# Kernel tuning notes

Hardware: AMD Instinct MI355X
Metric: run time of the kernel (lower is better)

The kernel has to match this reference:

```python
import jax, jax.numpy as jnp
import numpy as np
from jax import lax

H = 65  # hidden size

def lstm_layer(x, w_ih, w_hh, b_ih, b_hh):
    # x: [B, T, in]; w_ih: [4H, in]; w_hh: [4H, H]; PyTorch gate order i,f,g,o
    B = x.shape[0]
    # precompute input contribution for all timesteps: [T, B, 4H]
    pre = jnp.einsum('bti,gi->tbg', x, w_ih) + (b_ih + b_hh)
    wh = w_hh.T  # [H, 4H]

    def step(carry, pre_t):
        h, c = carry
        gates = pre_t + h @ wh
        i, f, g, o = jnp.split(gates, 4, axis=-1)
        i = jax.nn.sigmoid(i)
        f = jax.nn.sigmoid(f)
        g = jnp.tanh(g)
        o = jax.nn.sigmoid(o)
        c = f * c + i * g
        h = o * jnp.tanh(c)
        return (h, c), h

    init = (jnp.zeros((B, H), x.dtype), jnp.zeros((B, H), x.dtype))
    _, hs = lax.scan(step, init, pre)  # hs: [T, B, H]
    return jnp.transpose(hs, (1, 0, 2))  # [B, T, H]


def setup_inputs() -> dict:
    key = jax.random.key(0)
    ks = jax.random.split(key, 11)
    B, T = 512, 1024
    s = 1.0 / np.sqrt(H)
    d = {
        'x': jax.random.normal(ks[0], (B, T, H), jnp.float32),
        'w_ih0': jax.random.normal(ks[1], (4 * H, H), jnp.float32) * s,
        'w_hh0': jax.random.normal(ks[2], (4 * H, H), jnp.float32) * s,
        'b_ih0': jax.random.normal(ks[3], (4 * H,), jnp.float32) * s,
        'b_hh0': jax.random.normal(ks[4], (4 * H,), jnp.float32) * s,
        'w_ih1': jax.random.normal(ks[5], (4 * H, H), jnp.float32) * s,
        'w_hh1': jax.random.normal(ks[6], (4 * H, H), jnp.float32) * s,
        'b_ih1': jax.random.normal(ks[7], (4 * H,), jnp.float32) * s,
        'b_hh1': jax.random.normal(ks[8], (4 * H,), jnp.float32) * s,
        'w_lin': jax.random.normal(ks[9], (1, H), jnp.float32) * s,
        'b_lin': jax.random.normal(ks[10], (1,), jnp.float32) * s,
    }
    return d


def reference(x, w_ih0, w_hh0, b_ih0, b_hh0, w_ih1, w_hh1, b_ih1, b_hh1, w_lin, b_lin):
    h1 = lstm_layer(x, w_ih0, w_hh0, b_ih0, b_hh0)   # [B, T, H]
    h2 = lstm_layer(h1, w_ih1, w_hh1, b_ih1, b_hh1)  # [B, T, H]
    last = h2[:, -1, :]                               # [B, H]
    return last @ w_lin.T + b_lin                     # [B, 1]
```

## Files before the change

### kernel.cpp

```cpp
#include <hip/hip_runtime.h>

#define H 65
#define T_STEPS 1024

typedef _Float16 half_t;
typedef _Float16 half2_t __attribute__((ext_vector_type(2)));

static __device__ __forceinline__ float dot2(half2_t a, half2_t b, float c) {
#if __has_builtin(__builtin_amdgcn_fdot2)
  return __builtin_amdgcn_fdot2(a, b, c, false);
#else
  float d;
  asm("v_dot2_f32_f16 %0, %1, %2, %3" : "=v"(d) : "v"(a), "v"(b), "v"(c));
  return d;
#endif
}

template <int CTRL>
static __device__ __forceinline__ float qperm(float v) {
  int r = __builtin_amdgcn_update_dpp(0, __builtin_bit_cast(int, v), CTRL, 0xF, 0xF, true);
  return __builtin_bit_cast(float, r);
}

template <int PAT>
static __device__ __forceinline__ float swz(float v) {
  int r = __builtin_amdgcn_ds_swizzle(__builtin_bit_cast(int, v), PAT);
  return __builtin_bit_cast(float, r);
}

#define LOG2E 1.44269504089f
static __device__ __forceinline__ float fast_sigm(float v) {
  float e = __builtin_amdgcn_exp2f(-LOG2E * v);
  return __builtin_amdgcn_rcpf(1.f + e);
}

static __device__ __forceinline__ float pick(int idx, float a, float b, float c, float d) {
  float lo = (idx & 1) ? b : a;
  float hi = (idx & 1) ? d : c;
  return (idx & 2) ? hi : lo;
}

__global__
__attribute__((amdgpu_flat_work_group_size(1024, 1024)))
__attribute__((amdgpu_waves_per_eu(4, 4)))
void lstm_fused(
    const float* __restrict__ x,
    const float* __restrict__ wih0, const float* __restrict__ whh0,
    const float* __restrict__ bih0, const float* __restrict__ bhh0,
    const float* __restrict__ wih1, const float* __restrict__ whh1,
    const float* __restrict__ bih1, const float* __restrict__ bhh1,
    const float* __restrict__ wlin, const float* __restrict__ blin,
    float* __restrict__ out)
{
  __shared__ __align__(16) half_t xh[2][2][2][144];
  __shared__ float h1f[2][H];

  const int tid = threadIdx.x;
  const int rr  = tid >> 9;
  const int t5  = tid & 511;
  const int b   = 2 * blockIdx.x + rr;

  const int quad = t5 >> 2;
  const int l  = (quad >= 65) ? 1 : 0;
  const int j  = quad - 65 * l;
  const int kh = (t5 >> 1) & 1;
  const int g0 = t5 & 1;
  const bool gz = (g0 == 0);
  const float mreg = gz ? 2.f : 1.f;
  const float msub = mreg - 1.f;

  half2_t w[2][33];
  float hb[2];
  {
    const float* wi = l ? wih1 : wih0;
    const float* wh = l ? whh1 : whh0;
    const float* bi = l ? bih1 : bih0;
    const float* bh = l ? bhh1 : bhh0;
#pragma unroll
    for (int cc = 0; cc < 2; ++cc) {
      const int row = (g0 + 2 * cc) * H + j;
      hb[cc] = 0.5f * (bi[row] + bh[row]);
      const float* src = (kh ? wh : wi) + row * H;
#pragma unroll
      for (int pp = 0; pp < 33; ++pp) {
        float e0 = src[2 * pp];
        float e1 = (2 * pp + 1 < H) ? src[2 * pp + 1] : 0.f;
        half2_t v = {(half_t)e0, (half_t)e1};
        w[cc][pp] = v;
      }
    }
  }

  const bool isW7 = (t5 >= 448);
  const int  w7   = t5 - 448;
  const int  ec   = w7 >> 3;
  const int  ck   = w7 & 7;
  const int  side = ck >> 2;
  const int  sck  = ck & 3;
  const int  ecoff = side * 144 + 36 * sck;
  half2_t ecw[9];
  float ecbias = 0.f;
  float cec = 0.f;
  if (isW7) {
    const int gec = ec & 3;
    const int jec = 63 + (ec >> 2);
    const int row = gec * H + jec;
    const float* src = (side ? whh1 : wih1) + row * H;
#pragma unroll
    for (int i = 0; i < 9; ++i) {
      int es = 9 * sck + i;
      float e0 = (es < 33) ? src[2 * es] : 0.f;
      float e1 = (es < 33 && 2 * es + 1 < H) ? src[2 * es + 1] : 0.f;
      half2_t v = {(half_t)e0, (half_t)e1};
      ecw[i] = v;
    }
    if (ck == 0) ecbias = bih1[row] + bhh1[row];
  } else {
#pragma unroll
    for (int i = 0; i < 9; ++i) {
      half2_t z = {(half_t)0.f, (half_t)0.f};
      ecw[i] = z;
    }
  }

  const bool isW6 = (t5 >= 384) && (t5 < 448);
  const int  u    = t5 - 384;

  for (int i = tid; i < 2 * 2 * 2 * 144; i += 1024) ((half_t*)xh)[i] = (half_t)0.f;
  __syncthreads();

  const float* xrow = x + (size_t)b * (size_t)(T_STEPS * H);
  float nxA = 0.f, nxB = 0.f;
  if (isW6) {
    xh[rr][0][0][u] = (half_t)xrow[u];
    if (u == 0) xh[rr][0][0][64] = (half_t)xrow[64];
    nxA = xrow[H + u];
    if (u == 0) nxB = xrow[H + 64];
  }
  __syncthreads();

  float cst = 0.f;

  for (int s = 0; s <= T_STEPS; ++s) {
    const int p = s & 1;

    float fA = 0.f, fB = 0.f;
    if (isW6 && (s + 2 < T_STEPS)) {
      const float* xr = xrow + (size_t)(s + 2) * H;
      fA = xr[u];
      if (u == 0) fB = xr[64];
    }

    const bool act = l ? (s >= 1) : (s < T_STEPS);
    if (act) {
      const half_t* xb = &xh[rr][l][p][0] + 72 * kh;
      float a0 = hb[0], a1 = hb[1];
#pragma unroll
      for (int c = 0; c < 8; ++c) {
        uint4 qv = ((const uint4*)xb)[c];
        half2_t x0 = __builtin_bit_cast(half2_t, qv.x);
        half2_t x1 = __builtin_bit_cast(half2_t, qv.y);
        half2_t x2 = __builtin_bit_cast(half2_t, qv.z);
        half2_t x3 = __builtin_bit_cast(half2_t, qv.w);
        a0 = dot2(x0, w[0][4 * c + 0], a0);
        a1 = dot2(x0, w[1][4 * c + 0], a1);
        a0 = dot2(x1, w[0][4 * c + 1], a0);
        a1 = dot2(x1, w[1][4 * c + 1], a1);
        a0 = dot2(x2, w[0][4 * c + 2], a0);
        a1 = dot2(x2, w[1][4 * c + 2], a1);
        a0 = dot2(x3, w[0][4 * c + 3], a0);
        a1 = dot2(x3, w[1][4 * c + 3], a1);
      }
      {
        half2_t xt = *(const half2_t*)(xb + 64);
        a0 = dot2(xt, w[0][32], a0);
        a1 = dot2(xt, w[1][32], a1);
      }
      a0 += qperm<0x4E>(a0);
      a1 += qperm<0x4E>(a1);
      float e0 = fast_sigm(a0);
      float e1 = mreg * fast_sigm(mreg * a1) - msub;
      float p0 = qperm<0xB1>(e0);
      float p1 = qperm<0xB1>(e1);
      float iv = gz ? e0 : p0;
      float fv = gz ? p0 : e0;
      float gv = gz ? e1 : p1;
      float ov = gz ? p1 : e1;
      cst = fv * cst + iv * gv;
      float th = 2.f * fast_sigm(2.f * cst) - 1.f;
      float hv = ov * th;
      if ((t5 & 3) == 0) {
        half_t hh = (half_t)hv;
        if (l == 0) {
          xh[rr][0][p ^ 1][72 + j] = hh;
          xh[rr][1][p ^ 1][j]      = hh;
        } else {
          xh[rr][1][p ^ 1][72 + j] = hh;
          if (s == T_STEPS) h1f[rr][j] = hv;
        }
      }
    }

    if (isW7 && s >= 1) {
      const char* xb1 = (const char*)&xh[rr][1][p][0];
      float aec = ecbias;
#pragma unroll
      for (int i = 0; i < 9; ++i) {
        unsigned qv = *(const unsigned*)(xb1 + ecoff + 4 * i);
        aec = dot2(__builtin_bit_cast(half2_t, qv), ecw[i], aec);
      }
      aec += swz<0x041F>(aec);
      aec += swz<0x081F>(aec);
      aec += swz<0x101F>(aec);
      const int gec = ec & 3;
      float me = (gec == 2) ? 2.f : 1.f;
      float A  = me * fast_sigm(me * aec) - (me - 1.f);
      float Bv = swz<0x201F>(A);
      float Cv = swz<0x401F>(A);
      float Dv = swz<0x401F>(Bv);
      float iv2 = pick(gec ^ 0, A, Bv, Cv, Dv);
      float fv2 = pick(gec ^ 1, A, Bv, Cv, Dv);
      float gv2 = pick(gec ^ 2, A, Bv, Cv, Dv);
      float ov2 = pick(gec ^ 3, A, Bv, Cv, Dv);
      cec = fv2 * cec + iv2 * gv2;
      float hec = ov2 * (2.f * fast_sigm(2.f * cec) - 1.f);
      if (ck == 0 && (ec & 3) == 0) {
        const int jec = 63 + (ec >> 2);
        xh[rr][1][p ^ 1][72 + jec] = (half_t)hec;
        if (s == T_STEPS) h1f[rr][jec] = hec;
      }
    }

    if (isW6 && (s + 1 < T_STEPS)) {
      half_t* dst = &xh[rr][0][p ^ 1][0];
      dst[u] = (half_t)nxA;
      if (u == 0) dst[64] = (half_t)nxB;
      nxA = fA; nxB = fB;
    }
    __syncthreads();
  }

  if (t5 == 0) {
    float acc = blin[0];
    for (int jj = 0; jj < H; ++jj) acc += h1f[rr][jj] * wlin[jj];
    out[b] = acc;
  }
}

extern "C" void kernel_launch(void* const* d_in, const int* in_sizes, int n_in,
                              void* d_out, int out_size, void* d_ws, size_t ws_size,
                              hipStream_t stream) {
  const float* x    = (const float*)d_in[0];
  const float* wih0 = (const float*)d_in[1];
  const float* whh0 = (const float*)d_in[2];
  const float* bih0 = (const float*)d_in[3];
  const float* bhh0 = (const float*)d_in[4];
  const float* wih1 = (const float*)d_in[5];
  const float* whh1 = (const float*)d_in[6];
  const float* bih1 = (const float*)d_in[7];
  const float* bhh1 = (const float*)d_in[8];
  const float* wlin = (const float*)d_in[9];
  const float* blin = (const float*)d_in[10];
  float* out = (float*)d_out;

  lstm_fused<<<256, 1024, 0, stream>>>(x, wih0, whh0, bih0, bhh0,
                                       wih1, whh1, bih1, bhh1, wlin, blin, out);
}
```

Measured before the change: 1.461 ms.

## Add 512-thread two-batch LSTM variant with runtime fallback on register spills

The 1024-thread kernel drops its waves_per_eu bound and instead requests a fixed VGPR budget. A new 512-thread kernel has each thread process both batch rows of the block, reusing its register-resident weights across the two rows. At first launch the host queries the 1024-thread kernel's attributes and falls back to the 512-thread variant if it spills to scratch or has too few registers. This aims to avoid spill-induced slowdowns, at the cost of doubled per-thread serial work in the fallback path.

```diff
diff --git a/kernel.cpp b/kernel.cpp
--- a/kernel.cpp
+++ b/kernel.cpp
@@ -40,10 +40,16 @@
   return (idx & 2) ? hi : lo;
 }
 
+#if __has_attribute(amdgpu_num_vgpr)
+#define VGPR_REQ __attribute__((amdgpu_num_vgpr(120)))
+#else
+#define VGPR_REQ
+#endif
+
 __global__
 __attribute__((amdgpu_flat_work_group_size(1024, 1024)))
-__attribute__((amdgpu_waves_per_eu(4, 4)))
-void lstm_fused(
+VGPR_REQ
+void lstm_fused_1024(
     const float* __restrict__ x,
     const float* __restrict__ wih0, const float* __restrict__ whh0,
     const float* __restrict__ bih0, const float* __restrict__ bhh0,
@@ -247,6 +253,253 @@
   }
 }
 
+__global__ __launch_bounds__(512, 1) void lstm_fused_512(
+    const float* __restrict__ x,
+    const float* __restrict__ wih0, const float* __restrict__ whh0,
+    const float* __restrict__ bih0, const float* __restrict__ bhh0,
+    const float* __restrict__ wih1, const float* __restrict__ whh1,
+    const float* __restrict__ bih1, const float* __restrict__ bhh1,
+    const float* __restrict__ wlin, const float* __restrict__ blin,
+    float* __restrict__ out)
+{
+  __shared__ __align__(16) half_t xh[2][2][2][144];
+  __shared__ float h1f[2][H];
+
+  const int tid = threadIdx.x;
+
+  const int quad = tid >> 2;
+  const int l  = (quad >= 65) ? 1 : 0;
+  const int j  = quad - 65 * l;
+  const int kh = (tid >> 1) & 1;
+  const int g0 = tid & 1;
+  const bool gz = (g0 == 0);
+  const float mreg = gz ? 2.f : 1.f;
+  const float msub = mreg - 1.f;
+
+  half2_t w[2][33];
+  float hb[2];
+  {
+    const float* wi = l ? wih1 : wih0;
+    const float* wh = l ? whh1 : whh0;
+    const float* bi = l ? bih1 : bih0;
+    const float* bh = l ? bhh1 : bhh0;
+#pragma unroll
+    for (int cc = 0; cc < 2; ++cc) {
+      const int row = (g0 + 2 * cc) * H + j;
+      hb[cc] = 0.5f * (bi[row] + bh[row]);
+      const float* src = (kh ? wh : wi) + row * H;
+#pragma unroll
+      for (int pp = 0; pp < 33; ++pp) {
+        float e0 = src[2 * pp];
+        float e1 = (2 * pp + 1 < H) ? src[2 * pp + 1] : 0.f;
+        half2_t v = {(half_t)e0, (half_t)e1};
+        w[cc][pp] = v;
+      }
+    }
+  }
+
+  const bool isEC = (tid >= 384);
+  const int  e6   = tid & 63;
+  const int  ecR  = (tid >> 6) & 1;
+  const int  ec   = e6 >> 3;
+  const int  ck   = e6 & 7;
+  const int  side = ck >> 2;
+  const int  sck  = ck & 3;
+  const int  ecoff = side * 144 + 36 * sck;
+  half2_t ecw[9];
+  float ecbias = 0.f;
+  float cec = 0.f;
+  if (isEC) {
+    const int gec = ec & 3;
+    const int jec = 63 + (ec >> 2);
+    const int row = gec * H + jec;
+    const float* src = (side ? whh1 : wih1) + row * H;
+#pragma unroll
+    for (int i = 0; i < 9; ++i) {
+      int es = 9 * sck + i;
+      float e0 = (es < 33) ? src[2 * es] : 0.f;
+      float e1 = (es < 33 && 2 * es + 1 < H) ? src[2 * es + 1] : 0.f;
+      half2_t v = {(half_t)e0, (half_t)e1};
+      ecw[i] = v;
+    }
+    if (ck == 0) ecbias = bih1[row] + bhh1[row];
+  } else {
+#pragma unroll
+    for (int i = 0; i < 9; ++i) {
+      half2_t z = {(half_t)0.f, (half_t)0.f};
+      ecw[i] = z;
+    }
+  }
+
+  const bool isST = (tid < 64);
+  const int  u    = tid;
+
+  for (int i = tid; i < 2 * 2 * 2 * 144; i += 512) ((half_t*)xh)[i] = (half_t)0.f;
+  __syncthreads();
+
+  const float* xrowA = x + (size_t)(2 * blockIdx.x)     * (size_t)(T_STEPS * H);
+  const float* xrowB = x + (size_t)(2 * blockIdx.x + 1) * (size_t)(T_STEPS * H);
+  float nA = 0.f, nA64 = 0.f, nB = 0.f, nB64 = 0.f;
+  if (isST) {
+    xh[0][0][0][u] = (half_t)xrowA[u];
+    xh[1][0][0][u] = (half_t)xrowB[u];
+    if (u == 0) {
+      xh[0][0][0][64] = (half_t)xrowA[64];
+      xh[1][0][0][64] = (half_t)xrowB[64];
+    }
+    nA = xrowA[H + u];
+    nB = xrowB[H + u];
+    if (u == 0) { nA64 = xrowA[H + 64]; nB64 = xrowB[H + 64]; }
+  }
+  __syncthreads();
+
+  float cstA = 0.f, cstB = 0.f;
+
+  for (int s = 0; s <= T_STEPS; ++s) {
+    const int p = s & 1;
+
+    float fA = 0.f, fA64 = 0.f, fB = 0.f, fB64 = 0.f;
+    if (isST && (s + 2 < T_STEPS)) {
+      const float* xrA = xrowA + (size_t)(s + 2) * H;
+      const float* xrB = xrowB + (size_t)(s + 2) * H;
+      fA = xrA[u];
+      fB = xrB[u];
+      if (u == 0) { fA64 = xrA[64]; fB64 = xrB[64]; }
+    }
+
+    const bool act = l ? (s >= 1) : (s < T_STEPS);
+    if (act) {
+      const half_t* xbA = &xh[0][l][p][0] + 72 * kh;
+      const half_t* xbB = &xh[1][l][p][0] + 72 * kh;
+      float a0A = hb[0], a1A = hb[1];
+      float a0B = hb[0], a1B = hb[1];
+#pragma unroll
+      for (int c = 0; c < 8; ++c) {
+        uint4 qA = ((const uint4*)xbA)[c];
+        uint4 qB = ((const uint4*)xbB)[c];
+        half2_t xA0 = __builtin_bit_cast(half2_t, qA.x);
+        half2_t xA1 = __builtin_bit_cast(half2_t, qA.y);
+        half2_t xA2 = __builtin_bit_cast(half2_t, qA.z);
+        half2_t xA3 = __builtin_bit_cast(half2_t, qA.w);
+        half2_t xB0 = __builtin_bit_cast(half2_t, qB.x);
+        half2_t xB1 = __builtin_bit_cast(half2_t, qB.y);
+        half2_t xB2 = __builtin_bit_cast(half2_t, qB.z);
+        half2_t xB3 = __builtin_bit_cast(half2_t, qB.w);
+        a0A = dot2(xA0, w[0][4 * c + 0], a0A);
+        a0B = dot2(xB0, w[0][4 * c + 0], a0B);
+        a1A = dot2(xA0, w[1][4 * c + 0], a1A);
+        a1B = dot2(xB0, w[1][4 * c + 0], a1B);
+        a0A = dot2(xA1, w[0][4 * c + 1], a0A);
+        a0B = dot2(xB1, w[0][4 * c + 1], a0B);
+        a1A = dot2(xA1, w[1][4 * c + 1], a1A);
+        a1B = dot2(xB1, w[1][4 * c + 1], a1B);
+        a0A = dot2(xA2, w[0][4 * c + 2], a0A);
+        a0B = dot2(xB2, w[0][4 * c + 2], a0B);
+        a1A = dot2(xA2, w[1][4 * c + 2], a1A);
+        a1B = dot2(xB2, w[1][4 * c + 2], a1B);
+        a0A = dot2(xA3, w[0][4 * c + 3], a0A);
+        a0B = dot2(xB3, w[0][4 * c + 3], a0B);
+        a1A = dot2(xA3, w[1][4 * c + 3], a1A);
+        a1B = dot2(xB3, w[1][4 * c + 3], a1B);
+      }
+      {
+        half2_t xtA = *(const half2_t*)(xbA + 64);
+        half2_t xtB = *(const half2_t*)(xbB + 64);
+        a0A = dot2(xtA, w[0][32], a0A);
+        a0B = dot2(xtB, w[0][32], a0B);
+        a1A = dot2(xtA, w[1][32], a1A);
+        a1B = dot2(xtB, w[1][32], a1B);
+      }
+      a0A += qperm<0x4E>(a0A);
+      a1A += qperm<0x4E>(a1A);
+      a0B += qperm<0x4E>(a0B);
+      a1B += qperm<0x4E>(a1B);
+      float e0A = fast_sigm(a0A);
+      float e1A = mreg * fast_sigm(mreg * a1A) - msub;
+      float e0B = fast_sigm(a0B);
+      float e1B = mreg * fast_sigm(mreg * a1B) - msub;
+      float p0A = qperm<0xB1>(e0A);
+      float p1A = qperm<0xB1>(e1A);
+      float p0B = qperm<0xB1>(e0B);
+      float p1B = qperm<0xB1>(e1B);
+      float ivA = gz ? e0A : p0A, fvA = gz ? p0A : e0A;
+      float gvA = gz ? e1A : p1A, ovA = gz ? p1A : e1A;
+      float ivB = gz ? e0B : p0B, fvB = gz ? p0B : e0B;
+      float gvB = gz ? e1B : p1B, ovB = gz ? p1B : e1B;
+      cstA = fvA * cstA + ivA * gvA;
+      cstB = fvB * cstB + ivB * gvB;
+      float thA = 2.f * fast_sigm(2.f * cstA) - 1.f;
+      float thB = 2.f * fast_sigm(2.f * cstB) - 1.f;
+      float hvA = ovA * thA;
+      float hvB = ovB * thB;
+      if ((tid & 3) == 0) {
+        half_t hA = (half_t)hvA;
+        half_t hB = (half_t)hvB;
+        if (l == 0) {
+          xh[0][0][p ^ 1][72 + j] = hA;
+          xh[0][1][p ^ 1][j]      = hA;
+          xh[1][0][p ^ 1][72 + j] = hB;
+          xh[1][1][p ^ 1][j]      = hB;
+        } else {
+          xh[0][1][p ^ 1][72 + j] = hA;
+          xh[1][1][p ^ 1][72 + j] = hB;
+          if (s == T_STEPS) { h1f[0][j] = hvA; h1f[1][j] = hvB; }
+        }
+      }
+    }
+
+    if (isEC && s >= 1) {
+      const char* xb1 = (const char*)&xh[ecR][1][p][0];
+      float aec = ecbias;
+#pragma unroll
+      for (int i = 0; i < 9; ++i) {
+        unsigned qv = *(const unsigned*)(xb1 + ecoff + 4 * i);
+        aec = dot2(__builtin_bit_cast(half2_t, qv), ecw[i], aec);
+      }
+      aec += swz<0x041F>(aec);
+      aec += swz<0x081F>(aec);
+      aec += swz<0x101F>(aec);
+      const int gec = ec & 3;
+      float me = (gec == 2) ? 2.f : 1.f;
+      float A  = me * fast_sigm(me * aec) - (me - 1.f);
+      float Bv = swz<0x201F>(A);
+      float Cv = swz<0x401F>(A);
+      float Dv = swz<0x401F>(Bv);
+      float iv2 = pick(gec ^ 0, A, Bv, Cv, Dv);
+      float fv2 = pick(gec ^ 1, A, Bv, Cv, Dv);
+      float gv2 = pick(gec ^ 2, A, Bv, Cv, Dv);
+      float ov2 = pick(gec ^ 3, A, Bv, Cv, Dv);
+      cec = fv2 * cec + iv2 * gv2;
+      float hec = ov2 * (2.f * fast_sigm(2.f * cec) - 1.f);
+      if (ck == 0 && (ec & 3) == 0) {
+        const int jec = 63 + (ec >> 2);
+        xh[ecR][1][p ^ 1][72 + jec] = (half_t)hec;
+        if (s == T_STEPS) h1f[ecR][jec] = hec;
+      }
+    }
+
+    if (isST && (s + 1 < T_STEPS)) {
+      half_t* dA = &xh[0][0][p ^ 1][0];
+      half_t* dB = &xh[1][0][p ^ 1][0];
+      dA[u] = (half_t)nA;
+      dB[u] = (half_t)nB;
+      if (u == 0) { dA[64] = (half_t)nA64; dB[64] = (half_t)nB64; }
+      nA = fA; nA64 = fA64; nB = fB; nB64 = fB64;
+    }
+    __syncthreads();
+  }
+
+  if (tid == 0) {
+    float acc0 = blin[0], acc1 = blin[0];
+    for (int jj = 0; jj < H; ++jj) {
+      acc0 += h1f[0][jj] * wlin[jj];
+      acc1 += h1f[1][jj] * wlin[jj];
+    }
+    out[2 * blockIdx.x]     = acc0;
+    out[2 * blockIdx.x + 1] = acc1;
+  }
+}
+
 extern "C" void kernel_launch(void* const* d_in, const int* in_sizes, int n_in,
                               void* d_out, int out_size, void* d_ws, size_t ws_size,
                               hipStream_t stream) {
@@ -263,6 +516,22 @@
   const float* blin = (const float*)d_in[10];
   float* out = (float*)d_out;
 
-  lstm_fused<<<256, 1024, 0, stream>>>(x, wih0, whh0, bih0, bhh0,
-                                       wih1, whh1, bih1, bhh1, wlin, blin, out);
-}
+  static int use1024 = -1;
+  if (use1024 < 0) {
+    hipFuncAttributes a{};
+    if (hipFuncGetAttributes(&a, reinterpret_cast<const void*>(&lstm_fused_1024)) == hipSuccess &&
+        a.localSizeBytes == 0 && a.numRegs > 70) {
+      use1024 = 1;
+    } else {
+      use1024 = 0;
+    }
+  }
+
+  if (use1024) {
+    lstm_fused_1024<<<256, 1024, 0, stream>>>(x, wih0, whh0, bih0, bhh0,
+                                              wih1, whh1, bih1, bhh1, wlin, blin, out);
+  } else {
+    lstm_fused_512<<<256, 512, 0, stream>>>(x, wih0, whh0, bih0, bhh0,
+                                            wih1, whh1, bih1, bhh1, wlin, blin, out);
+  }
+}
```

After: 1.436 ms. No clear change (-1.7%).
